# Kernel optimization log

Hardware: AMD Instinct MI355X
Metric: run time of the kernel (lower is better)

Reference implementation:

```python
import jax, jax.numpy as jnp
import numpy as np

B, S, D, E = 4, 4096, 2048, 8
T = B * S                      # 16384 tokens
C = int(T / E * 1.25)          # capacity = 2560


def setup_inputs() -> dict:
    key = jax.random.key(0)
    k1, k2, k3 = jax.random.split(key, 3)
    rng = np.random.default_rng(0)
    # each token routed to one expert; overflow tokens beyond capacity are dropped
    expert_of = rng.integers(0, E, T)
    scatter_idx = np.full(E * C, T, dtype=np.int32)   # sentinel T -> dummy row
    dropped_mask = np.zeros(T, dtype=bool)
    for e in range(E):
        idx = np.nonzero(expert_of == e)[0]
        kept = idx[:C]
        scatter_idx[e * C: e * C + kept.size] = kept
        dropped_mask[idx[C:]] = True
    return {
        "expert_outputs": jax.random.normal(k1, (E * C, D), dtype=jnp.float32),
        "x": jax.random.normal(k2, (B, S, D), dtype=jnp.float32),
        "route_prob_max": jax.random.uniform(k3, (T,), dtype=jnp.float32),
        "scatter_idx": jnp.asarray(scatter_idx),
        "dropped_mask": jnp.asarray(dropped_mask),
    }


def reference(expert_outputs, x, route_prob_max, scatter_idx, dropped_mask):
    b, s, d = x.shape
    x_flat = x.reshape(-1, d)                         # [T, D]
    t = x_flat.shape[0]
    # scatter expert outputs to token positions; sentinel index t lands in dummy row
    buf = jnp.zeros((t + 1, d), dtype=x.dtype)
    final = buf.at[scatter_idx].set(expert_outputs)[:t]
    # dropped tokens pass through residual; their routing factor is 1.0
    final = jnp.where(dropped_mask[:, None], x_flat, final)
    factor = jnp.where(dropped_mask, jnp.asarray(1.0, x.dtype), route_prob_max)
    final = final * factor[:, None]
    return final.reshape(b, s, d)   # dropout p=0.0 -> identity
```

## Files before the change

kernel.cpp:

```cpp
#include <hip/hip_runtime.h>

__global__ void build_slot_kernel(const int* __restrict__ scatter_idx,
                                  int* __restrict__ slot, int n, int T) {
    int j = blockIdx.x * blockDim.x + threadIdx.x;
    if (j < n) {
        int t = scatter_idx[j];
        if ((unsigned)t < (unsigned)T) slot[t] = j + 1;
    }
}

__global__ void moe_out_kernel(const float4* __restrict__ eo,
                               const float4* __restrict__ x,
                               const float* __restrict__ rpm,
                               const int* __restrict__ slot,
                               float4* __restrict__ out, int D4) {
    int t = blockIdx.y;
    int c = blockIdx.x * blockDim.x + threadIdx.x;
    if (c >= D4) return;
    int s = slot[t];
    const float4* src;
    float f;
    if (s > 0) {
        src = eo + (size_t)(s - 1) * D4 + c;
        f = rpm[t];
    } else {
        src = x + (size_t)t * D4 + c;
        f = 1.0f;
    }
    float4 v = *src;
    v.x *= f; v.y *= f; v.z *= f; v.w *= f;
    out[(size_t)t * D4 + c] = v;
}

extern "C" void kernel_launch(void* const* d_in, const int* in_sizes, int n_in,
                              void* d_out, int out_size, void* d_ws, size_t ws_size,
                              hipStream_t stream) {
    const float* eo          = (const float*)d_in[0];
    const float* x           = (const float*)d_in[1];
    const float* rpm         = (const float*)d_in[2];
    const int*   scatter_idx = (const int*)d_in[3];

    const int T  = in_sizes[2];
    const int D  = in_sizes[1] / T;
    const int n  = in_sizes[3];
    const int D4 = D / 4;

    int* slot = (int*)d_ws;
    hipMemsetAsync(slot, 0, (size_t)T * sizeof(int), stream);

    build_slot_kernel<<<(n + 255) / 256, 256, 0, stream>>>(scatter_idx, slot, n, T);

    dim3 grid((D4 + 255) / 256, T);
    moe_out_kernel<<<grid, 256, 0, stream>>>(
        (const float4*)eo, (const float4*)x, rpm, slot, (float4*)d_out, D4);
}
```

Before: 320.6 us.

## Replace slot-map gather with direct scatter plus dropped-token passthrough in one kernel

Removes the memset and the slot-building kernel and launches a single kernel whose grid covers the expert rows plus the token rows. Expert rows scatter their scaled outputs straight to token positions, and token rows copy x only where dropped_mask is set. This cuts two launches and the dependent slot lookup, but the grid grows to n+T rows with many blocks that exit early. The new path reads dropped_mask and assumes every token is either scattered or marked dropped, and it drops the c<D4 bounds check.

```diff
diff --git a/kernel.cpp b/kernel.cpp
--- a/kernel.cpp
+++ b/kernel.cpp
@@ -1,56 +1,45 @@
 #include <hip/hip_runtime.h>
 
-__global__ void build_slot_kernel(const int* __restrict__ scatter_idx,
-                                  int* __restrict__ slot, int n, int T) {
-    int j = blockIdx.x * blockDim.x + threadIdx.x;
-    if (j < n) {
-        int t = scatter_idx[j];
-        if ((unsigned)t < (unsigned)T) slot[t] = j + 1;
+__global__ void moe_combine_kernel(const float4* __restrict__ eo,
+                                   const float4* __restrict__ x,
+                                   const float* __restrict__ rpm,
+                                   const int* __restrict__ scatter_idx,
+                                   const unsigned char* __restrict__ dropped,
+                                   float4* __restrict__ out,
+                                   int n, int T, int D4) {
+    int row = blockIdx.y;
+    int c = blockIdx.x * blockDim.x + threadIdx.x;
+
+    if (row < n) {
+        int t = scatter_idx[row];
+        if ((unsigned)t >= (unsigned)T) return;
+        float f = rpm[t];
+        float4 v = eo[(size_t)row * D4 + c];
+        v.x *= f; v.y *= f; v.z *= f; v.w *= f;
+        out[(size_t)t * D4 + c] = v;
+    } else {
+        int t = row - n;
+        if (!dropped[t]) return;
+        out[(size_t)t * D4 + c] = x[(size_t)t * D4 + c];
     }
-}
-
-__global__ void moe_out_kernel(const float4* __restrict__ eo,
-                               const float4* __restrict__ x,
-                               const float* __restrict__ rpm,
-                               const int* __restrict__ slot,
-                               float4* __restrict__ out, int D4) {
-    int t = blockIdx.y;
-    int c = blockIdx.x * blockDim.x + threadIdx.x;
-    if (c >= D4) return;
-    int s = slot[t];
-    const float4* src;
-    float f;
-    if (s > 0) {
-        src = eo + (size_t)(s - 1) * D4 + c;
-        f = rpm[t];
-    } else {
-        src = x + (size_t)t * D4 + c;
-        f = 1.0f;
-    }
-    float4 v = *src;
-    v.x *= f; v.y *= f; v.z *= f; v.w *= f;
-    out[(size_t)t * D4 + c] = v;
 }
 
 extern "C" void kernel_launch(void* const* d_in, const int* in_sizes, int n_in,
                               void* d_out, int out_size, void* d_ws, size_t ws_size,
                               hipStream_t stream) {
-    const float* eo          = (const float*)d_in[0];
-    const float* x           = (const float*)d_in[1];
-    const float* rpm         = (const float*)d_in[2];
-    const int*   scatter_idx = (const int*)d_in[3];
+    const float* eo            = (const float*)d_in[0];
+    const float* x             = (const float*)d_in[1];
+    const float* rpm           = (const float*)d_in[2];
+    const int*   scatter_idx   = (const int*)d_in[3];
+    const unsigned char* dmask = (const unsigned char*)d_in[4];
 
     const int T  = in_sizes[2];
     const int D  = in_sizes[1] / T;
     const int n  = in_sizes[3];
     const int D4 = D / 4;
 
-    int* slot = (int*)d_ws;
-    hipMemsetAsync(slot, 0, (size_t)T * sizeof(int), stream);
-
-    build_slot_kernel<<<(n + 255) / 256, 256, 0, stream>>>(scatter_idx, slot, n, T);
-
-    dim3 grid((D4 + 255) / 256, T);
-    moe_out_kernel<<<grid, 256, 0, stream>>>(
-        (const float4*)eo, (const float4*)x, rpm, slot, (float4*)d_out, D4);
+    dim3 grid((D4 + 255) / 256, n + T);
+    moe_combine_kernel<<<grid, 256, 0, stream>>>(
+        (const float4*)eo, (const float4*)x, rpm, scatter_idx, dmask,
+        (float4*)d_out, n, T, D4);
 }
```

Result: slower. 330.6 us (+3.1%).
